# Optimization experiments

Measured on AMD Instinct MI355X. Metric: run time of the kernel, lower is better.

## Reference

```python
import jax, jax.numpy as jnp
import numpy as np
from jax import lax

K = 3          # kernel_size
STRIDE = 2
BN_EPS = 1e-5
CLAMP_MIN = 1e-4


def setup_inputs() -> dict:
    key = jax.random.key(0)
    k1, k2 = jax.random.split(key)
    x = jax.random.normal(k1, (16, 64, 112, 112), dtype=jnp.float32)
    # kaiming-normal fan_out init: std = sqrt(2 / (out_ch * kh * kw))
    std = np.sqrt(2.0 / (9 * 3 * 3)).astype(np.float32)
    conv_w = jax.random.normal(k2, (9, 64, 3, 3), dtype=jnp.float32) * std
    gamma = jnp.ones((9,), dtype=jnp.float32)
    beta = jnp.zeros((9,), dtype=jnp.float32)
    return {"x": x, "conv_w": conv_w, "gamma": gamma, "beta": beta}


def reference(x, conv_w, gamma, beta):
    p = K // 2
    n, c, h, w = x.shape
    xp = jnp.pad(x, ((0, 0), (0, 0), (p, p), (p, p)), mode="reflect")  # [n,c,h+2p,w+2p]

    # sigma = BN(conv(pad(x))) with 3x3 conv, stride 1, no bias -> [n, k*k, h, w]
    sigma = lax.conv_general_dilated(
        xp, conv_w, window_strides=(1, 1), padding="VALID",
        dimension_numbers=("NCHW", "OIHW", "NCHW"))
    mean = jnp.mean(sigma, axis=(0, 2, 3), keepdims=True)
    var = jnp.var(sigma, axis=(0, 2, 3), keepdims=True)
    sigma = (sigma - mean) * lax.rsqrt(var + BN_EPS)
    sigma = sigma * gamma[None, :, None, None] + beta[None, :, None, None]
    sigma = jnp.clip(sigma, CLAMP_MIN)               # clamp(min=1e-4)
    sigma = sigma / jnp.sum(sigma, axis=1, keepdims=True)  # normalize over k*k taps

    # unfold pad(x) into k*k patches -> [n, c*k*k, h, w] (channel-major like torch unfold)
    patches = lax.conv_general_dilated_patches(
        xp, filter_shape=(K, K), window_strides=(1, 1), padding="VALID",
        dimension_numbers=("NCHW", "OIHW", "NCHW"))
    patches = patches.reshape(n, c, K * K, h, w)

    out = jnp.sum(patches * sigma[:, None], axis=2)  # [n, c, h, w]
    return out[:, :, ::STRIDE, ::STRIDE]
```

## Files before the change

### kernel.cpp

```cpp
#include <hip/hip_runtime.h>
#include <math.h>

namespace {

constexpr int Hh = 112, Ww = 112, Cc = 64, Nn = 16;
constexpr int OHh = 56, OWw = 56;
constexpr int HW = Hh * Ww;
constexpr int OP = OHh * OWw;
constexpr int NP = Nn * OP;
constexpr float BN_EPS_F = 1e-5f;
constexpr float CLAMP_MIN_F = 1e-4f;
constexpr int TP = 24;
constexpr int TE = 10 * 18;
constexpr int NSTAT = 16;
constexpr int CPW = Cc / 4;

__device__ __forceinline__ int reflect_idx(int t) {
    t = t < 0 ? -t : t;
    return (t >= Hh) ? (2 * Hh - 2 - t) : t;
}

__global__ __launch_bounds__(256) void conv_stats_sig_kernel(
    const float* __restrict__ x, const float* __restrict__ wgt,
    double* __restrict__ stats, float* __restrict__ sig_raw )
{
    __shared__ float tile[4][2][10 * TP];
    __shared__ float red[2][128][9];
    __shared__ float rsum[2][9], rsq[2][9];

    const int tid = threadIdx.x;
    const int lane = tid & 63;
    const int wv = __builtin_amdgcn_readfirstlane(tid >> 6);

    const int f = blockIdx.x;
    const int fs = (f & 7) * 196 + (f >> 3);
    const int t = fs % 98;
    const int n = fs / 98;
    const int h0 = (t / 7) * 8, w0 = (t % 7) * 16;

    int gg[3], ll[3];
#pragma unroll
    for (int s = 0; s < 3; ++s) {
        const int i = lane + 64 * s;
        const int r = i / 18, cl = i - r * 18;
        ll[s] = r * TP + cl;
        gg[s] = reflect_idx(h0 - 1 + r) * Ww + reflect_idx(w0 - 1 + cl);
    }
    const bool v2 = (lane < TE - 128);

    const float* xw = x + ((size_t)n * Cc + wv * CPW) * HW;
    float* myt0 = &tile[wv][0][0];
    float* myt1 = &tile[wv][1][0];

    myt0[ll[0]] = xw[gg[0]];
    myt0[ll[1]] = xw[gg[1]];
    if (v2) myt0[ll[2]] = xw[gg[2]];

    float acc[2][9];
#pragma unroll
    for (int u = 0; u < 2; ++u)
#pragma unroll
        for (int k = 0; k < 9; ++k) acc[u][k] = 0.f;

    const int px = lane & 15, py0 = lane >> 4;

#pragma unroll 2
    for (int c = 0; c < CPW; ++c) {
        float p0 = 0.f, p1 = 0.f, p2 = 0.f;
        if (c + 1 < CPW) {
            const float* xn = xw + (size_t)(c + 1) * HW;
            p0 = xn[gg[0]];
            p1 = xn[gg[1]];
            if (v2) p2 = xn[gg[2]];
        }

        const float* tl = (c & 1) ? myt1 : myt0;
        float xv[2][9];
#pragma unroll
        for (int u = 0; u < 2; ++u)
#pragma unroll
            for (int dy = 0; dy < 3; ++dy)
#pragma unroll
                for (int dx = 0; dx < 3; ++dx)
                    xv[u][dy * 3 + dx] = tl[(py0 + 4 * u + dy) * TP + (px + dx)];

        const int cg = wv * CPW + c;
#pragma unroll
        for (int k = 0; k < 9; ++k) {
            const float* wk = wgt + ((size_t)k * Cc + cg) * 9;
#pragma unroll
            for (int q = 0; q < 9; ++q) {
                const float w = wk[q];
                acc[0][k] = fmaf(w, xv[0][q], acc[0][k]);
                acc[1][k] = fmaf(w, xv[1][q], acc[1][k]);
            }
        }

        if (c + 1 < CPW) {
            float* td = ((c + 1) & 1) ? myt1 : myt0;
            td[ll[0]] = p0;
            td[ll[1]] = p1;
            if (v2) td[ll[2]] = p2;
        }
    }

#pragma unroll
    for (int u = 0; u < 2; ++u) {
        const int pix = (py0 + 4 * u) * 16 + px;
        if (wv >= 2) {
#pragma unroll
            for (int k = 0; k < 9; ++k) red[wv - 2][pix][k] = acc[u][k];
        }
    }
    __syncthreads();
#pragma unroll
    for (int u = 0; u < 2; ++u) {
        const int pix = (py0 + 4 * u) * 16 + px;
        if (wv < 2) {
#pragma unroll
            for (int k = 0; k < 9; ++k) red[wv][pix][k] += acc[u][k];
        }
    }
    __syncthreads();

    float sig[9];
    if (tid < 128) {
#pragma unroll
        for (int k = 0; k < 9; ++k) sig[k] = red[0][tid][k] + red[1][tid][k];

        const int pyt = tid >> 4, pxt = tid & 15;
        if (!(pyt & 1) && !(pxt & 1)) {
            const int oh = (h0 + pyt) >> 1, ow = (w0 + pxt) >> 1;
            const int pp = n * OP + oh * OWw + ow;
#pragma unroll
            for (int k = 0; k < 9; ++k) sig_raw[(size_t)k * NP + pp] = sig[k];
        }
    } else {
#pragma unroll
        for (int k = 0; k < 9; ++k) sig[k] = 0.f;
    }

#pragma unroll
    for (int k = 0; k < 9; ++k) {
        float s = sig[k], q = sig[k] * sig[k];
#pragma unroll
        for (int off = 32; off > 0; off >>= 1) {
            s += __shfl_down(s, off, 64);
            q += __shfl_down(q, off, 64);
        }
        if (wv < 2 && lane == 0) { rsum[wv][k] = s; rsq[wv][k] = q; }
    }
    __syncthreads();
    if (tid < 9) {
        const float s = rsum[0][tid] + rsum[1][tid];
        const float q = rsq[0][tid] + rsq[1][tid];
        double* st = stats + (size_t)(fs & (NSTAT - 1)) * 18;
        atomicAdd(&st[tid], (double)s);
        atomicAdd(&st[9 + tid], (double)q);
    }
}

__global__ __launch_bounds__(256) void apply_kernel(
    const float* __restrict__ x, const float* __restrict__ sig_raw,
    const float* __restrict__ gamma, const float* __restrict__ beta,
    const double* __restrict__ stats, float* __restrict__ out)
{
    __shared__ float srow[9][OWw];
    __shared__ float mean_s[9], istd_s[9], gb[18];

    const int tid = threadIdx.x;
    const int f = blockIdx.x;
    const int fs = (f & 7) * 112 + (f >> 3);
    const int n = fs / OHh;
    const int oh = fs % OHh;

    if (tid < 9) {
        double s = 0.0, q = 0.0;
        for (int r = 0; r < NSTAT; ++r) { s += stats[r * 18 + tid]; q += stats[r * 18 + 9 + tid]; }
        const double cnt = (double)Nn * HW;
        const double m = s / cnt;
        const double v = q / cnt - m * m;
        mean_s[tid] = (float)m;
        istd_s[tid] = (float)(1.0 / sqrt(v + (double)BN_EPS_F));
        gb[tid] = gamma[tid];
        gb[9 + tid] = beta[tid];
    }
    __syncthreads();

    if (tid < OWw) {
        const int pp = n * OP + oh * OWw + tid;
        float s[9], ssum = 0.f;
#pragma unroll
        for (int k = 0; k < 9; ++k) {
            float v = fmaf((sig_raw[(size_t)k * NP + pp] - mean_s[k]) * istd_s[k], gb[k], gb[9 + k]);
            v = fmaxf(v, CLAMP_MIN_F);
            s[k] = v;
            ssum += v;
        }
        const float inv = 1.f / ssum;
#pragma unroll
        for (int k = 0; k < 9; ++k) srow[k][tid] = s[k] * inv;
    }
    __syncthreads();

    const int csub = tid >> 6;
    const int lane = tid & 63;
    if (lane >= OWw) return;
    const int ow = lane;

    const int r0 = (oh == 0) ? 1 : (2 * oh - 1);
    const int r1 = 2 * oh, r2 = 2 * oh + 1;
    const int c0 = (ow == 0) ? 1 : (2 * ow - 1);
    const int c1 = 2 * ow, c2 = 2 * ow + 1;

    float sg[9];
#pragma unroll
    for (int k = 0; k < 9; ++k) sg[k] = srow[k][ow];

#pragma unroll 2
    for (int cc = 0; cc < 16; ++cc) {
        const int c = cc * 4 + csub;
        const float* xc = x + ((size_t)(n * Cc + c)) * HW;
        float o = 0.f;
        o = fmaf(sg[0], xc[r0 * Ww + c0], o);
        o = fmaf(sg[1], xc[r0 * Ww + c1], o);
        o = fmaf(sg[2], xc[r0 * Ww + c2], o);
        o = fmaf(sg[3], xc[r1 * Ww + c0], o);
        o = fmaf(sg[4], xc[r1 * Ww + c1], o);
        o = fmaf(sg[5], xc[r1 * Ww + c2], o);
        o = fmaf(sg[6], xc[r2 * Ww + c0], o);
        o = fmaf(sg[7], xc[r2 * Ww + c1], o);
        o = fmaf(sg[8], xc[r2 * Ww + c2], o);
        out[((size_t)(n * Cc + c)) * OP + oh * OWw + ow] = o;
    }
}

}

extern "C" void kernel_launch(void* const* d_in, const int* in_sizes, int n_in,
                              void* d_out, int out_size, void* d_ws, size_t ws_size,
                              hipStream_t stream) {
    const float* x     = (const float*)d_in[0];
    const float* wgt   = (const float*)d_in[1];
    const float* gamma = (const float*)d_in[2];
    const float* beta  = (const float*)d_in[3];
    float* out = (float*)d_out;

    double* stats  = (double*)d_ws;
    float* sig_raw = (float*)((char*)d_ws + 4096);

    hipMemsetAsync(d_ws, 0, 4096, stream);
    conv_stats_sig_kernel<<<1568, 256, 0, stream>>>(x, wgt, stats, sig_raw);
    apply_kernel<<<896, 256, 0, stream>>>(x, sig_raw, gamma, beta, stats, out);
}
```

Before: 85.22 us.

## Split conv by channel halves with per-pixel threads and separate merge/stats kernel

Replaces the LDS-tiled conv+stats kernel with a per-pixel conv kernel that splits the channels into two halves and writes full-resolution partial sigma maps. A new merge kernel sums the halves, computes the BN statistics over all pixels, and extracts the even-pixel sigma. This raises parallelism and removes the LDS tiling and in-block reductions, at the cost of a large intermediate buffer round-tripping through memory and an extra kernel launch.

Measured after the change: 82.73 us. 1.03x faster.

```diff
diff --git a/kernel.cpp b/kernel.cpp
--- a/kernel.cpp
+++ b/kernel.cpp
@@ -8,155 +8,97 @@
 constexpr int HW = Hh * Ww;
 constexpr int OP = OHh * OWw;
 constexpr int NP = Nn * OP;
+constexpr int NHW = Nn * HW;
 constexpr float BN_EPS_F = 1e-5f;
 constexpr float CLAMP_MIN_F = 1e-4f;
-constexpr int TP = 24;
-constexpr int TE = 10 * 18;
-constexpr int NSTAT = 16;
-constexpr int CPW = Cc / 4;
+constexpr int NSTAT = 32;
+constexpr int CH = 32;
 
-__device__ __forceinline__ int reflect_idx(int t) {
-    t = t < 0 ? -t : t;
-    return (t >= Hh) ? (2 * Hh - 2 - t) : t;
-}
+__global__ __launch_bounds__(256) void conv_half_kernel(
+    const float* __restrict__ x, const float* __restrict__ wgt,
+    float* __restrict__ P)
+{
+    const int tid = threadIdx.x;
+    const int b = blockIdx.x;
+    const int swz = (b & 7) * 196 + (b >> 3);
+    const int half = swz / 784;
+    const int bid = swz - half * 784;
 
-__global__ __launch_bounds__(256) void conv_stats_sig_kernel(
-    const float* __restrict__ x, const float* __restrict__ wgt,
-    double* __restrict__ stats, float* __restrict__ sig_raw )
-{
-    __shared__ float tile[4][2][10 * TP];
-    __shared__ float red[2][128][9];
-    __shared__ float rsum[2][9], rsq[2][9];
+    const int pos = bid * 256 + tid;
+    const int n = bid / 49;
+    const int hw = pos - n * HW;
+    const int h = hw / Ww, w = hw - h * Ww;
 
-    const int tid = threadIdx.x;
-    const int lane = tid & 63;
-    const int wv = __builtin_amdgcn_readfirstlane(tid >> 6);
+    const int hm = (h == 0) ? 1 : (h - 1);
+    const int hp = (h == Hh - 1) ? (Hh - 2) : (h + 1);
+    const int wm = (w == 0) ? 1 : (w - 1);
+    const int wp = (w == Ww - 1) ? (Ww - 2) : (w + 1);
+    const int r0 = hm * Ww, r1 = h * Ww, r2 = hp * Ww;
 
-    const int f = blockIdx.x;
-    const int fs = (f & 7) * 196 + (f >> 3);
-    const int t = fs % 98;
-    const int n = fs / 98;
-    const int h0 = (t / 7) * 8, w0 = (t % 7) * 16;
+    int off[9];
+    off[0] = r0 + wm; off[1] = r0 + w; off[2] = r0 + wp;
+    off[3] = r1 + wm; off[4] = r1 + w; off[5] = r1 + wp;
+    off[6] = r2 + wm; off[7] = r2 + w; off[8] = r2 + wp;
 
-    int gg[3], ll[3];
+    const float* xb = x + ((size_t)n * Cc + half * CH) * HW;
+
+    float cur[9], nxt[9], acc[9];
 #pragma unroll
-    for (int s = 0; s < 3; ++s) {
-        const int i = lane + 64 * s;
-        const int r = i / 18, cl = i - r * 18;
-        ll[s] = r * TP + cl;
-        gg[s] = reflect_idx(h0 - 1 + r) * Ww + reflect_idx(w0 - 1 + cl);
-    }
-    const bool v2 = (lane < TE - 128);
-
-    const float* xw = x + ((size_t)n * Cc + wv * CPW) * HW;
-    float* myt0 = &tile[wv][0][0];
-    float* myt1 = &tile[wv][1][0];
-
-    myt0[ll[0]] = xw[gg[0]];
-    myt0[ll[1]] = xw[gg[1]];
-    if (v2) myt0[ll[2]] = xw[gg[2]];
-
-    float acc[2][9];
-#pragma unroll
-    for (int u = 0; u < 2; ++u)
-#pragma unroll
-        for (int k = 0; k < 9; ++k) acc[u][k] = 0.f;
-
-    const int px = lane & 15, py0 = lane >> 4;
+    for (int j = 0; j < 9; ++j) { cur[j] = xb[off[j]]; acc[j] = 0.f; }
 
 #pragma unroll 2
-    for (int c = 0; c < CPW; ++c) {
-        float p0 = 0.f, p1 = 0.f, p2 = 0.f;
-        if (c + 1 < CPW) {
-            const float* xn = xw + (size_t)(c + 1) * HW;
-            p0 = xn[gg[0]];
-            p1 = xn[gg[1]];
-            if (v2) p2 = xn[gg[2]];
-        }
+    for (int c = 0; c < CH; ++c) {
+        const float* xn = xb + (size_t)((c + 1) & (CH - 1)) * HW;
+#pragma unroll
+        for (int j = 0; j < 9; ++j) nxt[j] = xn[off[j]];
 
-        const float* tl = (c & 1) ? myt1 : myt0;
-        float xv[2][9];
-#pragma unroll
-        for (int u = 0; u < 2; ++u)
-#pragma unroll
-            for (int dy = 0; dy < 3; ++dy)
-#pragma unroll
-                for (int dx = 0; dx < 3; ++dx)
-                    xv[u][dy * 3 + dx] = tl[(py0 + 4 * u + dy) * TP + (px + dx)];
-
-        const int cg = wv * CPW + c;
+        const int cg = half * CH + c;
 #pragma unroll
         for (int k = 0; k < 9; ++k) {
             const float* wk = wgt + ((size_t)k * Cc + cg) * 9;
 #pragma unroll
-            for (int q = 0; q < 9; ++q) {
-                const float w = wk[q];
-                acc[0][k] = fmaf(w, xv[0][q], acc[0][k]);
-                acc[1][k] = fmaf(w, xv[1][q], acc[1][k]);
-            }
+            for (int q = 0; q < 9; ++q)
+                acc[k] = fmaf(wk[q], cur[q], acc[k]);
         }
-
-        if (c + 1 < CPW) {
-            float* td = ((c + 1) & 1) ? myt1 : myt0;
-            td[ll[0]] = p0;
-            td[ll[1]] = p1;
-            if (v2) td[ll[2]] = p2;
-        }
+#pragma unroll
+        for (int j = 0; j < 9; ++j) cur[j] = nxt[j];
     }
 
+    float* Ph = P + (size_t)half * 9 * NHW;
 #pragma unroll
-    for (int u = 0; u < 2; ++u) {
-        const int pix = (py0 + 4 * u) * 16 + px;
-        if (wv >= 2) {
+    for (int k = 0; k < 9; ++k) Ph[(size_t)k * NHW + pos] = acc[k];
+}
+
+__global__ __launch_bounds__(256) void merge_stats_kernel(
+    const float* __restrict__ P, double* __restrict__ stats,
+    float* __restrict__ sig_even )
+{
+    __shared__ float rs[4], rq[4];
+    const int tid = threadIdx.x;
+    const int k = blockIdx.y;
+    const int p = blockIdx.x * 256 + tid;
+
+    const float v = P[(size_t)k * NHW + p] + P[(size_t)(9 + k) * NHW + p];
+
+    const int w = p % Ww;
+    const int h = (p / Ww) % Hh;
+    const int n = p / HW;
+    if (!(w & 1) && !(h & 1))
+        sig_even[(size_t)k * NP + n * OP + (h >> 1) * OWw + (w >> 1)] = v;
+
+    float s = v, q = v * v;
 #pragma unroll
-            for (int k = 0; k < 9; ++k) red[wv - 2][pix][k] = acc[u][k];
-        }
+    for (int off = 32; off > 0; off >>= 1) {
+        s += __shfl_down(s, off, 64);
+        q += __shfl_down(q, off, 64);
     }
+    const int lane = tid & 63, wv = tid >> 6;
+    if (lane == 0) { rs[wv] = s; rq[wv] = q; }
     __syncthreads();
-#pragma unroll
-    for (int u = 0; u < 2; ++u) {
-        const int pix = (py0 + 4 * u) * 16 + px;
-        if (wv < 2) {
-#pragma unroll
-            for (int k = 0; k < 9; ++k) red[wv][pix][k] += acc[u][k];
-        }
-    }
-    __syncthreads();
-
-    float sig[9];
-    if (tid < 128) {
-#pragma unroll
-        for (int k = 0; k < 9; ++k) sig[k] = red[0][tid][k] + red[1][tid][k];
-
-        const int pyt = tid >> 4, pxt = tid & 15;
-        if (!(pyt & 1) && !(pxt & 1)) {
-            const int oh = (h0 + pyt) >> 1, ow = (w0 + pxt) >> 1;
-            const int pp = n * OP + oh * OWw + ow;
-#pragma unroll
-            for (int k = 0; k < 9; ++k) sig_raw[(size_t)k * NP + pp] = sig[k];
-        }
-    } else {
-#pragma unroll
-        for (int k = 0; k < 9; ++k) sig[k] = 0.f;
-    }
-
-#pragma unroll
-    for (int k = 0; k < 9; ++k) {
-        float s = sig[k], q = sig[k] * sig[k];
-#pragma unroll
-        for (int off = 32; off > 0; off >>= 1) {
-            s += __shfl_down(s, off, 64);
-            q += __shfl_down(q, off, 64);
-        }
-        if (wv < 2 && lane == 0) { rsum[wv][k] = s; rsq[wv][k] = q; }
-    }
-    __syncthreads();
-    if (tid < 9) {
-        const float s = rsum[0][tid] + rsum[1][tid];
-        const float q = rsq[0][tid] + rsq[1][tid];
-        double* st = stats + (size_t)(fs & (NSTAT - 1)) * 18;
-        atomicAdd(&st[tid], (double)s);
-        atomicAdd(&st[9 + tid], (double)q);
+    if (tid == 0) {
+        double* st = stats + (size_t)(blockIdx.x & (NSTAT - 1)) * 18;
+        atomicAdd(&st[k], (double)(rs[0] + rs[1] + rs[2] + rs[3]));
+        atomicAdd(&st[9 + k], (double)(rq[0] + rq[1] + rq[2] + rq[3]));
     }
 }
 
@@ -246,10 +188,12 @@
     const float* beta  = (const float*)d_in[3];
     float* out = (float*)d_out;
 
-    double* stats  = (double*)d_ws;
-    float* sig_raw = (float*)((char*)d_ws + 4096);
+    double* stats = (double*)d_ws;
+    float* P        = (float*)((char*)d_ws + 8192);
+    float* sig_even = P + (size_t)18 * NHW;
 
-    hipMemsetAsync(d_ws, 0, 4096, stream);
-    conv_stats_sig_kernel<<<1568, 256, 0, stream>>>(x, wgt, stats, sig_raw);
-    apply_kernel<<<896, 256, 0, stream>>>(x, sig_raw, gamma, beta, stats, out);
+    hipMemsetAsync(d_ws, 0, 8192, stream);
+    conv_half_kernel<<<1568, 256, 0, stream>>>(x, wgt, P);
+    merge_stats_kernel<<<dim3(NHW / 256, 9), 256, 0, stream>>>(P, stats, sig_even);
+    apply_kernel<<<896, 256, 0, stream>>>(x, sig_even, gamma, beta, stats, out);
 }
```
